# Optimization experiments

Hardware: AMD Instinct MI355X
Metric: run time of the kernel (lower is better)

## Reference

```python
import jax, jax.numpy as jnp
import numpy as np

# Norse default LIFParameters
TAU_SYN_INV = 200.0  # 1/5e-3
TAU_MEM_INV = 100.0  # 1/1e-2
V_LEAK = 0.0
V_TH = 1.0
V_RESET = 0.0
DT = 0.001


def _heaviside(x):
    return (x > 0).astype(x.dtype)


def setup_inputs() -> dict:
    key = jax.random.key(0)
    k1, k2 = jax.random.split(key)
    T, B, F = 1024, 256, 512
    input_spikes = (jax.random.uniform(k1, (T, B, F)) < 0.1).astype(jnp.float32)
    W = jax.random.normal(k2, (F, F), dtype=jnp.float32) / np.sqrt(F).astype(np.float32)
    return {"input_spikes": input_spikes, "W": W}


def reference(input_spikes, W):
    # input_spikes: [T, B, F]; W: [F, F] (Linear, no bias)
    T, B, F = input_spikes.shape
    # fc batched across the whole sequence (y = x @ W.T)
    xs = jnp.einsum('tbf,gf->tbg', input_spikes, W)  # [T, B, F]
    v0 = jnp.zeros((B, F), dtype=input_spikes.dtype)
    i0 = jnp.zeros((B, F), dtype=input_spikes.dtype)

    def step(carry, x):
        v, i = carry
        v_dec = v + DT * TAU_MEM_INV * ((V_LEAK - v) + i)  # membrane leak+integrate
        i_dec = i - DT * TAU_SYN_INV * i                   # synaptic current decay
        z = _heaviside(v_dec - V_TH)                       # spike
        v_new = (1.0 - z) * v_dec + z * V_RESET            # reset
        i_new = i_dec + x                                  # inject fc output
        return (v_new, i_new), z

    (v, i), zs = jax.lax.scan(step, (v0, i0), xs)
    # matches torch forward: returns (z_last, state) with state = (v, i)
    return zs[-1], v, i
```

## Files before the change

### kernel.cpp

```cpp
#include <hip/hip_runtime.h>
#include <hip/hip_bf16.h>


typedef __attribute__((ext_vector_type(8))) short short8;
typedef __attribute__((ext_vector_type(4))) float floatx4;
typedef __attribute__((ext_vector_type(2))) unsigned uintx2;
typedef __attribute__((ext_vector_type(4))) int int4v;

#define T_STEPS 1024
#define B_DIM   256
#define F_DIM   512
#define BF      (B_DIM * F_DIM)
#define ROWP    520

static __device__ __forceinline__ unsigned short f2bf_rne(float f) {
    unsigned u = __float_as_uint(f);
    return (unsigned short)((u + 0x7FFFu + ((u >> 16) & 1u)) >> 16);
}
static __device__ __forceinline__ float bf2f(unsigned short h) {
    return __uint_as_float(((unsigned)h) << 16);
}

__global__ __launch_bounds__(256)
void pack_kernel(const float* __restrict__ sp, unsigned* __restrict__ bits)
{
    const int lane = threadIdx.x & 63;
    const int wv   = blockIdx.x * 4 + (threadIdx.x >> 6);
    for (int c = wv; c < 65536; c += 2048 * 4) {
        const float* p = sp + (size_t)c * 2048;
        unsigned val = 0;
        #pragma unroll
        for (int r = 0; r < 32; ++r) {
            float x = p[r * 64 + lane];
            unsigned long long m = __ballot(x != 0.0f);
            unsigned sel = (lane & 1) ? (unsigned)(m >> 32) : (unsigned)m;
            if ((lane >> 1) == r) val = sel;
        }
        bits[(size_t)c * 64 + lane] = val;
    }
}

__global__ __launch_bounds__(512, 4)
void lif_kernel_bits(const unsigned* __restrict__ bits,
                     const float* __restrict__ W,
                     float* __restrict__ out)
{
    __shared__ float xbuf[2][7 * 256];
    __shared__ float rowmax[8][16];

    const int tid  = threadIdx.x;
    const int lane = tid & 63;
    const int wq   = tid >> 6;
    const int bt   = blockIdx.x & 15;
    const int gb   = blockIdx.x >> 4;
    const int b0   = bt * 16;
    const int gw   = gb * 16;
    const int mrow = lane & 15;
    const int lq   = lane >> 4;

    int4v wi0, wi1, wi2;
    float invC;
    {
        const float* wp = W + (size_t)(gw + mrow) * F_DIM + wq * 64 + lq * 16;
        float wv[16];
        float lm = 0.0f;
        #pragma unroll
        for (int j = 0; j < 16; ++j) {
            wv[j] = wp[j];
            lm = fmaxf(lm, fabsf(wv[j]));
        }
        lm = fmaxf(lm, __shfl_xor(lm, 16, 64));
        lm = fmaxf(lm, __shfl_xor(lm, 32, 64));
        if (lane < 16) rowmax[wq][lane] = lm;
        __syncthreads();
        float S = 1e-30f;
        #pragma unroll
        for (int w8 = 0; w8 < 8; ++w8) S = fmaxf(S, rowmax[w8][mrow]);
        __syncthreads();
        const float C = 8000000.0f / S;
        invC = S / 8000000.0f;
        #pragma unroll
        for (int d = 0; d < 4; ++d) {
            unsigned p0 = 0, p1 = 0, p2 = 0;
            #pragma unroll
            for (int jj = 0; jj < 4; ++jj) {
                int q  = __float2int_rn(wv[d * 4 + jj] * C);
                int d2 = (q << 24) >> 24;
                int r1 = (q - d2) >> 8;
                int d1 = (r1 << 24) >> 24;
                int d0 = (r1 - d1) >> 8;
                p0 |= (unsigned)(d0 & 0xFF) << (8 * jj);
                p1 |= (unsigned)(d1 & 0xFF) << (8 * jj);
                p2 |= (unsigned)(d2 & 0xFF) << (8 * jj);
            }
            wi0[d] = (int)p0; wi1[d] = (int)p1; wi2[d] = (int)p2;
        }
    }

    float v[4]  = {0.f, 0.f, 0.f, 0.f};
    float cu[4] = {0.f, 0.f, 0.f, 0.f};
    float zf[4] = {0.f, 0.f, 0.f, 0.f};

    const unsigned* bp = bits + (size_t)(b0 + mrow) * 16 + wq * 2;

    auto ldbits = [&](int t) -> uintx2 {
        return *(const uintx2*)(bp + (size_t)t * 4096);
    };

    auto expand = [&](uintx2 bq) -> int4v {
        unsigned h16 = ((lq & 2) ? bq[1] : bq[0]) >> ((lq & 1) * 16);
        int4v a;
        #pragma unroll
        for (int d = 0; d < 4; ++d) {
            unsigned b4 = (h16 >> (4 * d)) & 0xFu;
            unsigned u  = (b4 << 7) + b4;
            u = (b4 << 14) + u;
            u = (b4 << 21) + u;
            a[d] = (int)(u & 0x01010101u);
        }
        return a;
    };

    const int4v iz = {0, 0, 0, 0};

    auto mfma_combine = [&](int4v aI) -> floatx4 {
        int4v acc0 = __builtin_amdgcn_mfma_i32_16x16x64_i8(aI, wi0, iz, 0, 0, 0);
        int4v acc1 = __builtin_amdgcn_mfma_i32_16x16x64_i8(aI, wi1, iz, 0, 0, 0);
        int4v acc2 = __builtin_amdgcn_mfma_i32_16x16x64_i8(aI, wi2, iz, 0, 0, 0);
        floatx4 M;
        #pragma unroll
        for (int r = 0; r < 4; ++r) {
            int a12 = (acc1[r] << 8) + acc2[r];
            M[r] = fmaf((float)acc0[r], 65536.0f, (float)a12);
        }
        return M;
    };

    auto lif_step = [&](const floatx4& Mown, const float* xb) {
        floatx4 s = Mown;
        #pragma unroll
        for (int j = 0; j < 7; ++j) {
            floatx4 p = *(const floatx4*)(xb + j * 256 + lane * 4);
            #pragma unroll
            for (int r = 0; r < 4; ++r) s[r] += p[r];
        }
        #pragma unroll
        for (int r = 0; r < 4; ++r) {
            float x    = s[r] * invC;
            float vdec = v[r] + 0.1f * ((0.0f - v[r]) + cu[r]);
            float idec = cu[r] - 0.2f * cu[r];
            bool  spk  = (vdec - 1.0f) > 0.0f;
            zf[r] = spk ? 1.0f : 0.0f;
            v[r]  = spk ? 0.0f : vdec;
            cu[r] = idec + x;
        }
    };

    floatx4 MA = {0.f, 0.f, 0.f, 0.f};
    floatx4 MB = {0.f, 0.f, 0.f, 0.f};

    uintx2 bqA = ldbits(0);
    uintx2 bqB = ldbits(1);

    for (int t = 0; t < T_STEPS; t += 2) {
        if (wq == 0 && t > 0)
            lif_step(MB, &xbuf[1][0]);
        {
            int4v aI = expand(bqA);
            if (t + 2 < T_STEPS) bqA = ldbits(t + 2);
            floatx4 M = mfma_combine(aI);
            if (wq > 0) *(floatx4*)&xbuf[0][(wq - 1) * 256 + lane * 4] = M;
            else        MA = M;
        }
        __syncthreads();

        if (wq == 0)
            lif_step(MA, &xbuf[0][0]);
        {
            int4v aI = expand(bqB);
            if (t + 3 < T_STEPS) bqB = ldbits(t + 3);
            floatx4 M = mfma_combine(aI);
            if (wq > 0) *(floatx4*)&xbuf[1][(wq - 1) * 256 + lane * 4] = M;
            else        MB = M;
        }
        __syncthreads();
    }
    if (wq == 0) {
        lif_step(MB, &xbuf[1][0]);
        #pragma unroll
        for (int r = 0; r < 4; ++r) {
            const size_t idx = (size_t)(b0 + lq * 4 + r) * F_DIM + gw + mrow;
            out[idx]          = zf[r];
            out[BF + idx]     = v[r];
            out[2 * BF + idx] = cu[r];
        }
    }
}

__global__ __launch_bounds__(256, 1)
void lif_kernel_f32(const float* __restrict__ spikes,
                    const float* __restrict__ W,
                    float* __restrict__ out)
{
    __shared__ unsigned short sAf[16 * ROWP];
    __shared__ float xbuf[2 * 256];

    const int tid  = threadIdx.x;
    const int lane = tid & 63;
    const int w    = tid >> 6;
    const int gh   = w & 1;
    const int kh   = w >> 1;
    const int bt   = blockIdx.x & 15;
    const int gb   = blockIdx.x >> 4;
    const int b0   = bt * 16;
    const int gw   = gb * 32 + gh * 16;
    const int mrow = lane & 15;
    const int kq   = lane >> 4;

    short8 whi[8], wmd[8], wlo[8];
    {
        const float* wp = W + (size_t)(gw + mrow) * F_DIM + kh * 256 + kq * 8;
        #pragma unroll
        for (int ks = 0; ks < 8; ++ks) {
            short8 hi, md, lo;
            #pragma unroll
            for (int j = 0; j < 8; ++j) {
                float f = wp[ks * 32 + j];
                unsigned short h = f2bf_rne(f);
                float r1 = f - bf2f(h);
                unsigned short m = f2bf_rne(r1);
                float r2 = r1 - bf2f(m);
                hi[j] = (short)h;
                md[j] = (short)m;
                lo[j] = (short)f2bf_rne(r2);
            }
            whi[ks] = hi; wmd[ks] = md; wlo[ks] = lo;
        }
    }

    float v[4]  = {0.f, 0.f, 0.f, 0.f};
    float cu[4] = {0.f, 0.f, 0.f, 0.f};
    float zf[4] = {0.f, 0.f, 0.f, 0.f};

    floatx4 ld[8];
    auto issue_loads = [&](int t) {
        const floatx4* sp = (const floatx4*)(spikes + (size_t)t * BF + (size_t)b0 * F_DIM);
        #pragma unroll
        for (int j = 0; j < 8; ++j)
            ld[j] = sp[tid + 256 * j];
    };

    issue_loads(0);
    for (int t = 0; t < T_STEPS; ++t) {
        #pragma unroll
        for (int j = 0; j < 8; ++j) {
            const int q = tid + 256 * j;
            const int row = q >> 7, col4 = q & 127;
            unsigned u0 = __float_as_uint(ld[j][0]);
            unsigned u1 = __float_as_uint(ld[j][1]);
            unsigned u2 = __float_as_uint(ld[j][2]);
            unsigned u3 = __float_as_uint(ld[j][3]);
            uintx2 d;
            d[0] = (u0 >> 16) | (u1 & 0xFFFF0000u);
            d[1] = (u2 >> 16) | (u3 & 0xFFFF0000u);
            *(uintx2*)&sAf[row * ROWP + col4 * 4] = d;
        }
        __syncthreads();
        if (t + 1 < T_STEPS) issue_loads(t + 1);

        floatx4 ah = {0.f, 0.f, 0.f, 0.f};
        floatx4 am = {0.f, 0.f, 0.f, 0.f};
        floatx4 al = {0.f, 0.f, 0.f, 0.f};
        const unsigned short* arow = &sAf[mrow * ROWP + kh * 256 + kq * 8];
        #pragma unroll
        for (int ks = 0; ks < 8; ++ks) {
            short8 a = *(const short8*)(arow + ks * 32);
            ah = __builtin_amdgcn_mfma_f32_16x16x32_bf16(a, whi[ks], ah, 0, 0, 0);
            am = __builtin_amdgcn_mfma_f32_16x16x32_bf16(a, wmd[ks], am, 0, 0, 0);
            al = __builtin_amdgcn_mfma_f32_16x16x32_bf16(a, wlo[ks], al, 0, 0, 0);
        }

        if (kh == 1) {
            floatx4 xp = (ah + am) + al;
            *(floatx4*)&xbuf[gh * 256 + lane * 4] = xp;
        }
        __syncthreads();
        if (kh == 0) {
            floatx4 other = *(const floatx4*)&xbuf[gh * 256 + lane * 4];
            #pragma unroll
            for (int r = 0; r < 4; ++r) {
                float x    = ((ah[r] + am[r]) + al[r]) + other[r];
                float vdec = v[r] + 0.1f * ((0.0f - v[r]) + cu[r]);
                float idec = cu[r] - 0.2f * cu[r];
                bool  spk  = (vdec - 1.0f) > 0.0f;
                zf[r] = spk ? 1.0f : 0.0f;
                v[r]  = spk ? 0.0f : vdec;
                cu[r] = idec + x;
            }
        }
    }

    if (kh == 0) {
        #pragma unroll
        for (int r = 0; r < 4; ++r) {
            const size_t idx = (size_t)(b0 + kq * 4 + r) * F_DIM + gw + mrow;
            out[idx]          = zf[r];
            out[BF + idx]     = v[r];
            out[2 * BF + idx] = cu[r];
        }
    }
}

extern "C" void kernel_launch(void* const* d_in, const int* in_sizes, int n_in,
                              void* d_out, int out_size, void* d_ws, size_t ws_size,
                              hipStream_t stream)
{
    const float* spikes = (const float*)d_in[0];
    const float* W      = (const float*)d_in[1];
    float* out          = (float*)d_out;

    const size_t need = (size_t)T_STEPS * B_DIM * (F_DIM / 8);
    if (d_ws != nullptr && ws_size >= need) {
        unsigned* bits = (unsigned*)d_ws;
        pack_kernel<<<dim3(2048), dim3(256), 0, stream>>>(spikes, bits);
        lif_kernel_bits<<<dim3(512), dim3(512), 0, stream>>>(bits, W, out);
    } else {
        lif_kernel_f32<<<dim3(256), dim3(256), 0, stream>>>(spikes, W, out);
    }
}
```

Before: 1.147 ms.

## Pack spikes to int8 bytes instead of bits to skip in-loop expansion

Adds a pack kernel that converts the float spike tensor into one byte per element (0/1) using exponent-bit extraction, and a new LIF kernel that loads those int8 A-fragments directly for the i8 MFMA. This removes the per-step bit-to-byte expansion ALU work in the recurrent loop. In exchange, the intermediate buffer grows eightfold (128MB vs 16MB), adding pack-kernel write traffic and per-step read bandwidth. The new path runs only when the workspace is large enough.

```diff
diff --git a/kernel.cpp b/kernel.cpp
--- a/kernel.cpp
+++ b/kernel.cpp
@@ -5,6 +5,7 @@
 typedef __attribute__((ext_vector_type(8))) short short8;
 typedef __attribute__((ext_vector_type(4))) float floatx4;
 typedef __attribute__((ext_vector_type(2))) unsigned uintx2;
+typedef __attribute__((ext_vector_type(4))) unsigned uintx4;
 typedef __attribute__((ext_vector_type(4))) int int4v;
 
 #define T_STEPS 1024
@@ -19,6 +20,25 @@
 }
 static __device__ __forceinline__ float bf2f(unsigned short h) {
     return __uint_as_float(((unsigned)h) << 16);
+}
+
+__global__ __launch_bounds__(256)
+void pack_i8_kernel(const float* __restrict__ sp, uintx4* __restrict__ bytes)
+{
+    const size_t n16 = (size_t)T_STEPS * BF / 16;
+    for (size_t i = blockIdx.x * 256 + threadIdx.x; i < n16; i += 2048 * 256) {
+        const floatx4* p = (const floatx4*)(sp + i * 16);
+        uintx4 o;
+        #pragma unroll
+        for (int q = 0; q < 4; ++q) {
+            floatx4 f = p[q];
+            unsigned u0 = __float_as_uint(f[0]), u1 = __float_as_uint(f[1]);
+            unsigned u2 = __float_as_uint(f[2]), u3 = __float_as_uint(f[3]);
+            o[q] = ((u0 >> 23) & 1u)        | ((u1 >> 15) & 0x100u)
+                 | ((u2 >> 7)  & 0x10000u)  | ((u3 << 1)  & 0x1000000u);
+        }
+        bytes[i] = o;
+    }
 }
 
 __global__ __launch_bounds__(256)
@@ -40,10 +60,11 @@
     }
 }
 
+
 __global__ __launch_bounds__(512, 4)
-void lif_kernel_bits(const unsigned* __restrict__ bits,
-                     const float* __restrict__ W,
-                     float* __restrict__ out)
+void lif_kernel_i8(const unsigned char* __restrict__ a8,
+                   const float* __restrict__ W,
+                   float* __restrict__ out)
 {
     __shared__ float xbuf[2][7 * 256];
     __shared__ float rowmax[8][16];
@@ -101,6 +122,149 @@
     float cu[4] = {0.f, 0.f, 0.f, 0.f};
     float zf[4] = {0.f, 0.f, 0.f, 0.f};
 
+    const unsigned char* ap = a8 + (size_t)(b0 + mrow) * F_DIM + wq * 64 + lq * 16;
+
+    auto ldA = [&](int t) -> int4v {
+        return *(const int4v*)(ap + (size_t)t * BF);
+    };
+
+    const int4v iz = {0, 0, 0, 0};
+
+    auto mfma_combine = [&](int4v aI) -> floatx4 {
+        int4v acc0 = __builtin_amdgcn_mfma_i32_16x16x64_i8(aI, wi0, iz, 0, 0, 0);
+        int4v acc1 = __builtin_amdgcn_mfma_i32_16x16x64_i8(aI, wi1, iz, 0, 0, 0);
+        int4v acc2 = __builtin_amdgcn_mfma_i32_16x16x64_i8(aI, wi2, iz, 0, 0, 0);
+        floatx4 M;
+        #pragma unroll
+        for (int r = 0; r < 4; ++r) {
+            int a12 = (acc1[r] << 8) + acc2[r];
+            M[r] = fmaf((float)acc0[r], 65536.0f, (float)a12);
+        }
+        return M;
+    };
+
+    auto lif_step = [&](const floatx4& Mown, const float* xb) {
+        floatx4 s = Mown;
+        #pragma unroll
+        for (int j = 0; j < 7; ++j) {
+            floatx4 p = *(const floatx4*)(xb + j * 256 + lane * 4);
+            #pragma unroll
+            for (int r = 0; r < 4; ++r) s[r] += p[r];
+        }
+        #pragma unroll
+        for (int r = 0; r < 4; ++r) {
+            float x    = s[r] * invC;
+            float vdec = v[r] + 0.1f * ((0.0f - v[r]) + cu[r]);
+            float idec = cu[r] - 0.2f * cu[r];
+            bool  spk  = (vdec - 1.0f) > 0.0f;
+            zf[r] = spk ? 1.0f : 0.0f;
+            v[r]  = spk ? 0.0f : vdec;
+            cu[r] = idec + x;
+        }
+    };
+
+    floatx4 MA = {0.f, 0.f, 0.f, 0.f};
+    floatx4 MB = {0.f, 0.f, 0.f, 0.f};
+
+    int4v aA = ldA(0);
+    int4v aB = ldA(1);
+
+    for (int t = 0; t < T_STEPS; t += 2) {
+        if (wq == 0 && t > 0)
+            lif_step(MB, &xbuf[1][0]);
+        {
+            int4v aI = aA;
+            if (t + 2 < T_STEPS) aA = ldA(t + 2);
+            floatx4 M = mfma_combine(aI);
+            if (wq > 0) *(floatx4*)&xbuf[0][(wq - 1) * 256 + lane * 4] = M;
+            else        MA = M;
+        }
+        __syncthreads();
+
+        if (wq == 0)
+            lif_step(MA, &xbuf[0][0]);
+        {
+            int4v aI = aB;
+            if (t + 3 < T_STEPS) aB = ldA(t + 3);
+            floatx4 M = mfma_combine(aI);
+            if (wq > 0) *(floatx4*)&xbuf[1][(wq - 1) * 256 + lane * 4] = M;
+            else        MB = M;
+        }
+        __syncthreads();
+    }
+    if (wq == 0) {
+        lif_step(MB, &xbuf[1][0]);
+        #pragma unroll
+        for (int r = 0; r < 4; ++r) {
+            const size_t idx = (size_t)(b0 + lq * 4 + r) * F_DIM + gw + mrow;
+            out[idx]          = zf[r];
+            out[BF + idx]     = v[r];
+            out[2 * BF + idx] = cu[r];
+        }
+    }
+}
+
+__global__ __launch_bounds__(512, 4)
+void lif_kernel_bits(const unsigned* __restrict__ bits,
+                     const float* __restrict__ W,
+                     float* __restrict__ out)
+{
+    __shared__ float xbuf[2][7 * 256];
+    __shared__ float rowmax[8][16];
+
+    const int tid  = threadIdx.x;
+    const int lane = tid & 63;
+    const int wq   = tid >> 6;
+    const int bt   = blockIdx.x & 15;
+    const int gb   = blockIdx.x >> 4;
+    const int b0   = bt * 16;
+    const int gw   = gb * 16;
+    const int mrow = lane & 15;
+    const int lq   = lane >> 4;
+
+    int4v wi0, wi1, wi2;
+    float invC;
+    {
+        const float* wp = W + (size_t)(gw + mrow) * F_DIM + wq * 64 + lq * 16;
+        float wv[16];
+        float lm = 0.0f;
+        #pragma unroll
+        for (int j = 0; j < 16; ++j) {
+            wv[j] = wp[j];
+            lm = fmaxf(lm, fabsf(wv[j]));
+        }
+        lm = fmaxf(lm, __shfl_xor(lm, 16, 64));
+        lm = fmaxf(lm, __shfl_xor(lm, 32, 64));
+        if (lane < 16) rowmax[wq][lane] = lm;
+        __syncthreads();
+        float S = 1e-30f;
+        #pragma unroll
+        for (int w8 = 0; w8 < 8; ++w8) S = fmaxf(S, rowmax[w8][mrow]);
+        __syncthreads();
+        const float C = 8000000.0f / S;
+        invC = S / 8000000.0f;
+        #pragma unroll
+        for (int d = 0; d < 4; ++d) {
+            unsigned p0 = 0, p1 = 0, p2 = 0;
+            #pragma unroll
+            for (int jj = 0; jj < 4; ++jj) {
+                int q  = __float2int_rn(wv[d * 4 + jj] * C);
+                int d2 = (q << 24) >> 24;
+                int r1 = (q - d2) >> 8;
+                int d1 = (r1 << 24) >> 24;
+                int d0 = (r1 - d1) >> 8;
+                p0 |= (unsigned)(d0 & 0xFF) << (8 * jj);
+                p1 |= (unsigned)(d1 & 0xFF) << (8 * jj);
+                p2 |= (unsigned)(d2 & 0xFF) << (8 * jj);
+            }
+            wi0[d] = (int)p0; wi1[d] = (int)p1; wi2[d] = (int)p2;
+        }
+    }
+
+    float v[4]  = {0.f, 0.f, 0.f, 0.f};
+    float cu[4] = {0.f, 0.f, 0.f, 0.f};
+    float zf[4] = {0.f, 0.f, 0.f, 0.f};
+
     const unsigned* bp = bits + (size_t)(b0 + mrow) * 16 + wq * 2;
 
     auto ldbits = [&](int t) -> uintx2 {
@@ -319,8 +483,14 @@
     const float* W      = (const float*)d_in[1];
     float* out          = (float*)d_out;
 
-    const size_t need = (size_t)T_STEPS * B_DIM * (F_DIM / 8);
-    if (d_ws != nullptr && ws_size >= need) {
+    const size_t need_i8   = (size_t)T_STEPS * BF;
+    const size_t need_bits = (size_t)T_STEPS * B_DIM * (F_DIM / 8);
+
+    if (d_ws != nullptr && ws_size >= need_i8) {
+        unsigned char* a8 = (unsigned char*)d_ws;
+        pack_i8_kernel<<<dim3(2048), dim3(256), 0, stream>>>(spikes, (uintx4*)a8);
+        lif_kernel_i8<<<dim3(512), dim3(512), 0, stream>>>(a8, W, out);
+    } else if (d_ws != nullptr && ws_size >= need_bits) {
         unsigned* bits = (unsigned*)d_ws;
         pack_kernel<<<dim3(2048), dim3(256), 0, stream>>>(spikes, bits);
         lif_kernel_bits<<<dim3(512), dim3(512), 0, stream>>>(bits, W, out);
```

New measurement: 1.246 ms. 8.6% more time.

## Process two 16-column output tiles per block, reusing expanded spike bits

Applied to the files above, without the earlier changes.

Each block now covers 32 output columns instead of 16. It holds two sets of int8-split weight fragments and runs six MFMAs per timestep on the same expanded spike operand. The grid is halved to 256 blocks, and the LIF update for the second tile is handed to wave 1. Together these cut the bit loads, bit expansion and per-block barrier overhead relative to the work done. The bit expansion also becomes a single multiply, and the int accumulators are combined in integer arithmetic before conversion to float. In exchange the kernel uses more registers and LDS per block, has fewer blocks for latency hiding, and the integer combine could lose precision if sums exceed the float mantissa.

```diff
diff --git a/kernel.cpp b/kernel.cpp
--- a/kernel.cpp
+++ b/kernel.cpp
@@ -40,61 +40,69 @@
     }
 }
 
-__global__ __launch_bounds__(512, 4)
+__global__ __launch_bounds__(512, 2)
 void lif_kernel_bits(const unsigned* __restrict__ bits,
                      const float* __restrict__ W,
                      float* __restrict__ out)
 {
-    __shared__ float xbuf[2][7 * 256];
-    __shared__ float rowmax[8][16];
+    __shared__ float xbuf[2][2][7 * 256];
+    __shared__ float rowmax[8][32];
 
     const int tid  = threadIdx.x;
     const int lane = tid & 63;
     const int wq   = tid >> 6;
     const int bt   = blockIdx.x & 15;
-    const int gb   = blockIdx.x >> 4;
+    const int gb2  = blockIdx.x >> 4;
     const int b0   = bt * 16;
-    const int gw   = gb * 16;
+    const int gw   = gb2 * 32;
     const int mrow = lane & 15;
     const int lq   = lane >> 4;
 
-    int4v wi0, wi1, wi2;
-    float invC;
+    int4v wiA0, wiA1, wiA2, wiB0, wiB1, wiB2;
+    float invC0, invC1;
     {
-        const float* wp = W + (size_t)(gw + mrow) * F_DIM + wq * 64 + lq * 16;
-        float wv[16];
-        float lm = 0.0f;
-        #pragma unroll
-        for (int j = 0; j < 16; ++j) {
-            wv[j] = wp[j];
-            lm = fmaxf(lm, fabsf(wv[j]));
-        }
-        lm = fmaxf(lm, __shfl_xor(lm, 16, 64));
-        lm = fmaxf(lm, __shfl_xor(lm, 32, 64));
-        if (lane < 16) rowmax[wq][lane] = lm;
-        __syncthreads();
-        float S = 1e-30f;
-        #pragma unroll
-        for (int w8 = 0; w8 < 8; ++w8) S = fmaxf(S, rowmax[w8][mrow]);
-        __syncthreads();
-        const float C = 8000000.0f / S;
-        invC = S / 8000000.0f;
-        #pragma unroll
-        for (int d = 0; d < 4; ++d) {
-            unsigned p0 = 0, p1 = 0, p2 = 0;
-            #pragma unroll
-            for (int jj = 0; jj < 4; ++jj) {
-                int q  = __float2int_rn(wv[d * 4 + jj] * C);
-                int d2 = (q << 24) >> 24;
-                int r1 = (q - d2) >> 8;
-                int d1 = (r1 << 24) >> 24;
-                int d0 = (r1 - d1) >> 8;
-                p0 |= (unsigned)(d0 & 0xFF) << (8 * jj);
-                p1 |= (unsigned)(d1 & 0xFF) << (8 * jj);
-                p2 |= (unsigned)(d2 & 0xFF) << (8 * jj);
+        float wva[16], wvb[16];
+        auto loadmax = [&](int t2, float* wv) {
+            const float* wp = W + (size_t)(gw + t2 * 16 + mrow) * F_DIM + wq * 64 + lq * 16;
+            float lm = 0.0f;
+            #pragma unroll
+            for (int j = 0; j < 16; ++j) {
+                wv[j] = wp[j];
+                lm = fmaxf(lm, fabsf(wv[j]));
             }
-            wi0[d] = (int)p0; wi1[d] = (int)p1; wi2[d] = (int)p2;
-        }
+            lm = fmaxf(lm, __shfl_xor(lm, 16, 64));
+            lm = fmaxf(lm, __shfl_xor(lm, 32, 64));
+            if (lane < 16) rowmax[wq][t2 * 16 + lane] = lm;
+        };
+        loadmax(0, wva);
+        loadmax(1, wvb);
+        __syncthreads();
+        auto quant = [&](int t2, const float* wv, int4v& w0, int4v& w1, int4v& w2) -> float {
+            float S = 1e-30f;
+            #pragma unroll
+            for (int w8 = 0; w8 < 8; ++w8) S = fmaxf(S, rowmax[w8][t2 * 16 + mrow]);
+            const float C = 8000000.0f / S;
+            #pragma unroll
+            for (int d = 0; d < 4; ++d) {
+                unsigned p0 = 0, p1 = 0, p2 = 0;
+                #pragma unroll
+                for (int jj = 0; jj < 4; ++jj) {
+                    int q  = __float2int_rn(wv[d * 4 + jj] * C);
+                    int d2 = (q << 24) >> 24;
+                    int r1 = (q - d2) >> 8;
+                    int d1 = (r1 << 24) >> 24;
+                    int d0 = (r1 - d1) >> 8;
+                    p0 |= (unsigned)(d0 & 0xFF) << (8 * jj);
+                    p1 |= (unsigned)(d1 & 0xFF) << (8 * jj);
+                    p2 |= (unsigned)(d2 & 0xFF) << (8 * jj);
+                }
+                w0[d] = (int)p0; w1[d] = (int)p1; w2[d] = (int)p2;
+            }
+            return S / 8000000.0f;
+        };
+        invC0 = quant(0, wva, wiA0, wiA1, wiA2);
+        invC1 = quant(1, wvb, wiB0, wiB1, wiB2);
+        __syncthreads();
     }
 
     float v[4]  = {0.f, 0.f, 0.f, 0.f};
@@ -113,40 +121,44 @@
         #pragma unroll
         for (int d = 0; d < 4; ++d) {
             unsigned b4 = (h16 >> (4 * d)) & 0xFu;
-            unsigned u  = (b4 << 7) + b4;
-            u = (b4 << 14) + u;
-            u = (b4 << 21) + u;
-            a[d] = (int)(u & 0x01010101u);
+            a[d] = (int)((b4 * 0x00204081u) & 0x01010101u);
         }
         return a;
     };
 
     const int4v iz = {0, 0, 0, 0};
 
-    auto mfma_combine = [&](int4v aI) -> floatx4 {
-        int4v acc0 = __builtin_amdgcn_mfma_i32_16x16x64_i8(aI, wi0, iz, 0, 0, 0);
-        int4v acc1 = __builtin_amdgcn_mfma_i32_16x16x64_i8(aI, wi1, iz, 0, 0, 0);
-        int4v acc2 = __builtin_amdgcn_mfma_i32_16x16x64_i8(aI, wi2, iz, 0, 0, 0);
+    auto mc = [&](int4v aI, int4v w0, int4v w1, int4v w2) -> floatx4 {
+        int4v a0 = __builtin_amdgcn_mfma_i32_16x16x64_i8(aI, w0, iz, 0, 0, 0);
+        int4v a1 = __builtin_amdgcn_mfma_i32_16x16x64_i8(aI, w1, iz, 0, 0, 0);
+        int4v a2 = __builtin_amdgcn_mfma_i32_16x16x64_i8(aI, w2, iz, 0, 0, 0);
         floatx4 M;
         #pragma unroll
+        for (int r = 0; r < 4; ++r)
+            M[r] = (float)(((a0[r] << 16) + (a1[r] << 8)) + a2[r]);
+        return M;
+    };
+
+    auto lif_step = [&](floatx4 Mown, const float* xb, float ic, bool t1ord) {
+        floatx4 s;
+        int j0;
+        if (!t1ord) {
+            s = Mown;
+            j0 = 0;
+        } else {
+            s = *(const floatx4*)(xb + lane * 4);
+            #pragma unroll
+            for (int r = 0; r < 4; ++r) s[r] += Mown[r];
+            j0 = 1;
+        }
+        for (int j = j0; j < 7; ++j) {
+            floatx4 p = *(const floatx4*)(xb + j * 256 + lane * 4);
+            #pragma unroll
+            for (int r = 0; r < 4; ++r) s[r] += p[r];
+        }
+        #pragma unroll
         for (int r = 0; r < 4; ++r) {
-            int a12 = (acc1[r] << 8) + acc2[r];
-            M[r] = fmaf((float)acc0[r], 65536.0f, (float)a12);
-        }
-        return M;
-    };
-
-    auto lif_step = [&](const floatx4& Mown, const float* xb) {
-        floatx4 s = Mown;
-        #pragma unroll
-        for (int j = 0; j < 7; ++j) {
-            floatx4 p = *(const floatx4*)(xb + j * 256 + lane * 4);
-            #pragma unroll
-            for (int r = 0; r < 4; ++r) s[r] += p[r];
-        }
-        #pragma unroll
-        for (int r = 0; r < 4; ++r) {
-            float x    = s[r] * invC;
+            float x    = s[r] * ic;
             float vdec = v[r] + 0.1f * ((0.0f - v[r]) + cu[r]);
             float idec = cu[r] - 0.2f * cu[r];
             bool  spk  = (vdec - 1.0f) > 0.0f;
@@ -156,40 +168,51 @@
         }
     };
 
-    floatx4 MA = {0.f, 0.f, 0.f, 0.f};
-    floatx4 MB = {0.f, 0.f, 0.f, 0.f};
+    const int s0i = (wq - 1) * 256 + lane * 4;
+    const int s1i = ((wq == 0) ? 0 : (wq - 1)) * 256 + lane * 4;
+
+    const floatx4 fz = {0.f, 0.f, 0.f, 0.f};
+    floatx4 MA = fz, MB = fz;
 
     uintx2 bqA = ldbits(0);
     uintx2 bqB = ldbits(1);
 
     for (int t = 0; t < T_STEPS; t += 2) {
-        if (wq == 0 && t > 0)
-            lif_step(MB, &xbuf[1][0]);
+        if (t > 0) {
+            if (wq == 0)      lif_step(MB, &xbuf[1][0][0], invC0, false);
+            else if (wq == 1) lif_step(MB, &xbuf[1][1][0], invC1, true);
+        }
         {
             int4v aI = expand(bqA);
             if (t + 2 < T_STEPS) bqA = ldbits(t + 2);
-            floatx4 M = mfma_combine(aI);
-            if (wq > 0) *(floatx4*)&xbuf[0][(wq - 1) * 256 + lane * 4] = M;
-            else        MA = M;
-        }
-        __syncthreads();
-
-        if (wq == 0)
-            lif_step(MA, &xbuf[0][0]);
+            floatx4 M0 = mc(aI, wiA0, wiA1, wiA2);
+            floatx4 M1 = mc(aI, wiB0, wiB1, wiB2);
+            if (wq != 0) *(floatx4*)&xbuf[0][0][s0i] = M0;
+            if (wq != 1) *(floatx4*)&xbuf[0][1][s1i] = M1;
+            MA = (wq == 0) ? M0 : M1;
+        }
+        __syncthreads();
+
+        if (wq == 0)      lif_step(MA, &xbuf[0][0][0], invC0, false);
+        else if (wq == 1) lif_step(MA, &xbuf[0][1][0], invC1, true);
         {
             int4v aI = expand(bqB);
             if (t + 3 < T_STEPS) bqB = ldbits(t + 3);
-            floatx4 M = mfma_combine(aI);
-            if (wq > 0) *(floatx4*)&xbuf[1][(wq - 1) * 256 + lane * 4] = M;
-            else        MB = M;
-        }
-        __syncthreads();
-    }
-    if (wq == 0) {
-        lif_step(MB, &xbuf[1][0]);
+            floatx4 M0 = mc(aI, wiA0, wiA1, wiA2);
+            floatx4 M1 = mc(aI, wiB0, wiB1, wiB2);
+            if (wq != 0) *(floatx4*)&xbuf[1][0][s0i] = M0;
+            if (wq != 1) *(floatx4*)&xbuf[1][1][s1i] = M1;
+            MB = (wq == 0) ? M0 : M1;
+        }
+        __syncthreads();
+    }
+    if (wq == 0)      lif_step(MB, &xbuf[1][0][0], invC0, false);
+    else if (wq == 1) lif_step(MB, &xbuf[1][1][0], invC1, true);
+    if (wq < 2) {
+        const int gg = gw + wq * 16 + mrow;
         #pragma unroll
         for (int r = 0; r < 4; ++r) {
-            const size_t idx = (size_t)(b0 + lq * 4 + r) * F_DIM + gw + mrow;
+            const size_t idx = (size_t)(b0 + lq * 4 + r) * F_DIM + gg;
             out[idx]          = zf[r];
             out[BF + idx]     = v[r];
             out[2 * BF + idx] = cu[r];
@@ -319,11 +342,12 @@
     const float* W      = (const float*)d_in[1];
     float* out          = (float*)d_out;
 
-    const size_t need = (size_t)T_STEPS * B_DIM * (F_DIM / 8);
-    if (d_ws != nullptr && ws_size >= need) {
+    const size_t need_bits = (size_t)T_STEPS * B_DIM * (F_DIM / 8);
+
+    if (d_ws != nullptr && ws_size >= need_bits) {
         unsigned* bits = (unsigned*)d_ws;
         pack_kernel<<<dim3(2048), dim3(256), 0, stream>>>(spikes, bits);
-        lif_kernel_bits<<<dim3(512), dim3(512), 0, stream>>>(bits, W, out);
+        lif_kernel_bits<<<dim3(256), dim3(512), 0, stream>>>(bits, W, out);
     } else {
         lif_kernel_f32<<<dim3(256), dim3(256), 0, stream>>>(spikes, W, out);
     }
```

Result: no change. 1.160 ms (+1.1%).

## Process two timesteps per barrier with int partials and split LIF across two waves

Applied to the files above, without the earlier changes.

The LIF kernel now computes both timesteps' MFMA partials before a single barrier instead of one barrier per timestep. Partials are kept as combined integers in a 4-slot LDS ring, and the reduction plus LIF update is spread over two waves, each handling two rows. The recurrent update therefore runs one iteration behind the MFMA producers. This halves barrier count and moves some reduction work off a single wave. It increases LDS use and changes the float accumulation of the combine into integer addition, which may alter overflow or precision behaviour.

```diff
diff --git a/kernel.cpp b/kernel.cpp
--- a/kernel.cpp
+++ b/kernel.cpp
@@ -45,7 +45,7 @@
                      const float* __restrict__ W,
                      float* __restrict__ out)
 {
-    __shared__ float xbuf[2][7 * 256];
+    __shared__ int   xq[4][8 * 256];
     __shared__ float rowmax[8][16];
 
     const int tid  = threadIdx.x;
@@ -97,9 +97,9 @@
         }
     }
 
-    float v[4]  = {0.f, 0.f, 0.f, 0.f};
-    float cu[4] = {0.f, 0.f, 0.f, 0.f};
-    float zf[4] = {0.f, 0.f, 0.f, 0.f};
+    const bool fin   = (wq < 2);
+    const int  rbase = (wq & 1) * 2;
+    float v0 = 0.f, v1 = 0.f, c0 = 0.f, c1 = 0.f, z0 = 0.f, z1 = 0.f;
 
     const unsigned* bp = bits + (size_t)(b0 + mrow) * 16 + wq * 2;
 
@@ -113,86 +113,82 @@
         #pragma unroll
         for (int d = 0; d < 4; ++d) {
             unsigned b4 = (h16 >> (4 * d)) & 0xFu;
-            unsigned u  = (b4 << 7) + b4;
-            u = (b4 << 14) + u;
-            u = (b4 << 21) + u;
-            a[d] = (int)(u & 0x01010101u);
+            a[d] = (int)((b4 * 0x00204081u) & 0x01010101u);
         }
         return a;
     };
 
     const int4v iz = {0, 0, 0, 0};
 
-    auto mfma_combine = [&](int4v aI) -> floatx4 {
-        int4v acc0 = __builtin_amdgcn_mfma_i32_16x16x64_i8(aI, wi0, iz, 0, 0, 0);
-        int4v acc1 = __builtin_amdgcn_mfma_i32_16x16x64_i8(aI, wi1, iz, 0, 0, 0);
-        int4v acc2 = __builtin_amdgcn_mfma_i32_16x16x64_i8(aI, wi2, iz, 0, 0, 0);
-        floatx4 M;
-        #pragma unroll
-        for (int r = 0; r < 4; ++r) {
-            int a12 = (acc1[r] << 8) + acc2[r];
-            M[r] = fmaf((float)acc0[r], 65536.0f, (float)a12);
-        }
-        return M;
-    };
-
-    auto lif_step = [&](const floatx4& Mown, const float* xb) {
-        floatx4 s = Mown;
-        #pragma unroll
-        for (int j = 0; j < 7; ++j) {
-            floatx4 p = *(const floatx4*)(xb + j * 256 + lane * 4);
-            #pragma unroll
-            for (int r = 0; r < 4; ++r) s[r] += p[r];
-        }
-        #pragma unroll
-        for (int r = 0; r < 4; ++r) {
-            float x    = s[r] * invC;
-            float vdec = v[r] + 0.1f * ((0.0f - v[r]) + cu[r]);
-            float idec = cu[r] - 0.2f * cu[r];
-            bool  spk  = (vdec - 1.0f) > 0.0f;
-            zf[r] = spk ? 1.0f : 0.0f;
-            v[r]  = spk ? 0.0f : vdec;
-            cu[r] = idec + x;
-        }
-    };
-
-    floatx4 MA = {0.f, 0.f, 0.f, 0.f};
-    floatx4 MB = {0.f, 0.f, 0.f, 0.f};
+    auto mci = [&](int4v aI) -> int4v {
+        int4v a0 = __builtin_amdgcn_mfma_i32_16x16x64_i8(aI, wi0, iz, 0, 0, 0);
+        int4v a1 = __builtin_amdgcn_mfma_i32_16x16x64_i8(aI, wi1, iz, 0, 0, 0);
+        int4v a2 = __builtin_amdgcn_mfma_i32_16x16x64_i8(aI, wi2, iz, 0, 0, 0);
+        int4v c;
+        #pragma unroll
+        for (int r = 0; r < 4; ++r)
+            c[r] = ((a0[r] << 16) + (a1[r] << 8)) + a2[r];
+        return c;
+    };
+
+    auto lif2 = [&](const int* xs) {
+        int s0 = 0, s1 = 0;
+        #pragma unroll
+        for (int w8 = 0; w8 < 8; ++w8) {
+            const int* p = xs + w8 * 256 + lane * 4 + rbase;
+            s0 += p[0];
+            s1 += p[1];
+        }
+        float x0 = (float)s0 * invC;
+        float x1 = (float)s1 * invC;
+        float vd0 = v0 + 0.1f * ((0.0f - v0) + c0);
+        float id0 = c0 - 0.2f * c0;
+        bool  sp0 = (vd0 - 1.0f) > 0.0f;
+        z0 = sp0 ? 1.0f : 0.0f;
+        v0 = sp0 ? 0.0f : vd0;
+        c0 = id0 + x0;
+        float vd1 = v1 + 0.1f * ((0.0f - v1) + c1);
+        float id1 = c1 - 0.2f * c1;
+        bool  sp1 = (vd1 - 1.0f) > 0.0f;
+        z1 = sp1 ? 1.0f : 0.0f;
+        v1 = sp1 ? 0.0f : vd1;
+        c1 = id1 + x1;
+    };
 
     uintx2 bqA = ldbits(0);
     uintx2 bqB = ldbits(1);
 
     for (int t = 0; t < T_STEPS; t += 2) {
-        if (wq == 0 && t > 0)
-            lif_step(MB, &xbuf[1][0]);
+        if (fin && t > 0) {
+            lif2(&xq[(t + 2) & 3][0]);
+            lif2(&xq[(t + 3) & 3][0]);
+        }
         {
-            int4v aI = expand(bqA);
-            if (t + 2 < T_STEPS) bqA = ldbits(t + 2);
-            floatx4 M = mfma_combine(aI);
-            if (wq > 0) *(floatx4*)&xbuf[0][(wq - 1) * 256 + lane * 4] = M;
-            else        MA = M;
-        }
-        __syncthreads();
-
-        if (wq == 0)
-            lif_step(MA, &xbuf[0][0]);
+            int4v cA = mci(expand(bqA));
+            *(int4v*)&xq[t & 3][wq * 256 + lane * 4] = cA;
+            int4v cB = mci(expand(bqB));
+            *(int4v*)&xq[(t + 1) & 3][wq * 256 + lane * 4] = cB;
+        }
+        if (t + 2 < T_STEPS) {
+            bqA = ldbits(t + 2);
+            bqB = ldbits(t + 3);
+        }
+        __syncthreads();
+    }
+    if (fin) {
+        lif2(&xq[2][0]);
+        lif2(&xq[3][0]);
+        const int blo = b0 + lq * 4 + rbase;
+        const int gg  = gw + mrow;
         {
-            int4v aI = expand(bqB);
-            if (t + 3 < T_STEPS) bqB = ldbits(t + 3);
-            floatx4 M = mfma_combine(aI);
-            if (wq > 0) *(floatx4*)&xbuf[1][(wq - 1) * 256 + lane * 4] = M;
-            else        MB = M;
-        }
-        __syncthreads();
-    }
-    if (wq == 0) {
-        lif_step(MB, &xbuf[1][0]);
-        #pragma unroll
-        for (int r = 0; r < 4; ++r) {
-            const size_t idx = (size_t)(b0 + lq * 4 + r) * F_DIM + gw + mrow;
-            out[idx]          = zf[r];
-            out[BF + idx]     = v[r];
-            out[2 * BF + idx] = cu[r];
+            const size_t i0 = (size_t)blo * F_DIM + gg;
+            out[i0]          = z0;
+            out[BF + i0]     = v0;
+            out[2 * BF + i0] = c0;
+            const size_t i1 = (size_t)(blo + 1) * F_DIM + gg;
+            out[i1]          = z1;
+            out[BF + i1]     = v1;
+            out[2 * BF + i1] = c1;
         }
     }
 }
@@ -319,8 +315,9 @@
     const float* W      = (const float*)d_in[1];
     float* out          = (float*)d_out;
 
-    const size_t need = (size_t)T_STEPS * B_DIM * (F_DIM / 8);
-    if (d_ws != nullptr && ws_size >= need) {
+    const size_t need_bits = (size_t)T_STEPS * B_DIM * (F_DIM / 8);
+
+    if (d_ws != nullptr && ws_size >= need_bits) {
         unsigned* bits = (unsigned*)d_ws;
         pack_kernel<<<dim3(2048), dim3(256), 0, stream>>>(spikes, bits);
         lif_kernel_bits<<<dim3(512), dim3(512), 0, stream>>>(bits, W, out);
```

New measurement: 1.072 ms. 6.6% less time.
